# Kernel optimization log

Measured on AMD Instinct MI355X. Metric: run time of the kernel, lower is better.

## Reference

```python
import jax, jax.numpy as jnp
import numpy as np

B, C, T = 8, 1024, 2048
CI = C // 2
BN_EPS = 1e-5


def setup_inputs() -> dict:
    key = jax.random.key(0)
    ks = jax.random.split(key, 12)
    sc_in = 1.0 / np.sqrt(C)
    sc_ci = 1.0 / np.sqrt(CI)
    return {
        "x": jax.random.normal(ks[0], (B, C, T), dtype=jnp.float32),
        "Wq_w": jax.random.normal(ks[1], (CI, C), dtype=jnp.float32) * sc_in,
        "Wq_b": jax.random.normal(ks[2], (CI,), dtype=jnp.float32) * 0.02,
        "Wk_w": jax.random.normal(ks[3], (CI, C), dtype=jnp.float32) * sc_in,
        "Wk_b": jax.random.normal(ks[4], (CI,), dtype=jnp.float32) * 0.02,
        "Wv_w": jax.random.normal(ks[5], (CI, C), dtype=jnp.float32) * sc_in,
        "Wv_b": jax.random.normal(ks[6], (CI,), dtype=jnp.float32) * 0.02,
        "Wo_w": jax.random.normal(ks[7], (C, CI), dtype=jnp.float32) * sc_ci,
        "Wo_b": jax.random.normal(ks[8], (C,), dtype=jnp.float32) * 0.02,
        "gamma": jax.random.normal(ks[9], (C,), dtype=jnp.float32) * 0.1 + 1.0,
        "beta": jax.random.normal(ks[10], (C,), dtype=jnp.float32) * 0.02,
    }


def reference(x, Wq_w, Wq_b, Wk_w, Wk_b, Wv_w, Wv_b, Wo_w, Wo_b, gamma, beta):
    # 1x1 Conv1d projections == channel-wise linear maps
    q = jnp.einsum('oc,bct->bto', Wq_w, x) + Wq_b          # [B, T, Ci]
    k = jnp.einsum('oc,bct->bot', Wk_w, x) + Wk_b[:, None]  # [B, Ci, T]
    v = jnp.einsum('oc,bct->bto', Wv_w, x) + Wv_b          # [B, T, Ci]

    s = jnp.einsum('bqc,bck->bqk', q, k)                   # [B, Tq, Tk], unscaled
    sim = jax.nn.softmax(s, axis=-2)                        # softmax over QUERY axis
    y = jnp.einsum('bqk,bkc->bcq', sim, v)                  # [B, Ci, T]

    wy = jnp.einsum('oc,bct->bot', Wo_w, y) + Wo_b[:, None]  # [B, C, T]

    # BatchNorm1d in training mode: stats over (batch, time) per channel
    mean = jnp.mean(wy, axis=(0, 2), keepdims=True)
    var = jnp.var(wy, axis=(0, 2), keepdims=True)
    wy_bn = (wy - mean) * jax.lax.rsqrt(var + BN_EPS)
    wy_bn = wy_bn * gamma[None, :, None] + beta[None, :, None]

    return wy_bn + x
```

## Files before the change

kernel.cpp:

```cpp
#include <hip/hip_runtime.h>
#include <hip/hip_fp16.h>

typedef _Float16 f16;
typedef f16 f16x8 __attribute__((ext_vector_type(8)));
typedef f16 f16x4 __attribute__((ext_vector_type(4)));
typedef float f32x4 __attribute__((ext_vector_type(4)));

constexpr int Bb = 8, Cc = 1024, Tt = 2048, Ci = 512;
constexpr float BN_EPS = 1e-5f;

__device__ __forceinline__ void gload16(const f16* g, f16* l) {
  __builtin_amdgcn_global_load_lds(
      (const __attribute__((address_space(1))) void*)g,
      (__attribute__((address_space(3))) void*)l, 16, 0, 0);
}

__global__ __launch_bounds__(256)
void cvt_kernel(const float* __restrict__ src, f16* __restrict__ dst, int n4) {
  int i = blockIdx.x * blockDim.x + threadIdx.x;
  if (i < n4) {
    float4 v = *((const float4*)src + i);
    f16x4 h;
    h[0] = (f16)v.x; h[1] = (f16)v.y; h[2] = (f16)v.z; h[3] = (f16)v.w;
    *((f16x4*)dst + i) = h;
  }
}

__global__ __launch_bounds__(256)
void cvtT_kernel(const float* __restrict__ x, f16* __restrict__ xT) {
  __shared__ float tile[64][68];
  const int b = blockIdx.z, c0 = blockIdx.y * 64, t0 = blockIdx.x * 64;
  const int tid = threadIdx.x;
  const float* xp = x + ((long)b * Cc + c0) * Tt + t0;
  {
    int r = tid >> 4, c4 = (tid & 15) * 4;
    #pragma unroll
    for (int it = 0; it < 4; it++) {
      float4 v = *(const float4*)(xp + (long)(r + it * 16) * Tt + c4);
      *(float4*)&tile[r + it * 16][c4] = v;
    }
  }
  __syncthreads();
  f16* op = xT + ((long)b * Tt + t0) * Cc + c0;
  {
    int c8 = (tid & 7) * 8;
    #pragma unroll
    for (int it = 0; it < 2; it++) {
      int t = (tid >> 3) + it * 32;
      f16x8 o;
      #pragma unroll
      for (int jj = 0; jj < 8; jj++) o[jj] = (f16)tile[c8 + jj][t];
      *(f16x8*)(op + (long)t * Cc + c8) = o;
    }
  }
}

template<int BIAS_MODE, bool DO_MAX>
__device__ __forceinline__
void gemm_body(f16* lds, const f16* Ab, const f16* Bt, f16* C,
               const float* bias, unsigned* gmaxb,
               int K, int lda, int ldb, int ldc, int bm0, int bn0)
{
  constexpr int TILE_A = 256 * 32;
  constexpr int TILE_B = 128 * 32;
  constexpr int TILE   = TILE_A + TILE_B;

  const int tid = threadIdx.x, lane = tid & 63, wv = tid >> 6;
  const int wm = (wv >> 1) * 64, wn = (wv & 1) * 64;
  const int r16 = lane & 15, khi = lane >> 4;

  auto stA = [&](int slot, int k0, int r) {
    int L = (r * 512 + tid) * 16;
    int G = L ^ (((L >> 7) & 3) << 4);
    gload16(Ab + (long)(G >> 6) * lda + k0 + ((G & 63) >> 1),
            lds + (long)slot * TILE + (r * 512 + wv * 64) * 8);
  };
  auto stB = [&](int slot, int k0) {
    int L = tid * 16;
    int G = L ^ (((L >> 7) & 3) << 4);
    gload16(Bt + (long)(G >> 6) * ldb + k0 + ((G & 63) >> 1),
            lds + (long)slot * TILE + TILE_A + (wv * 64) * 8);
  };

  f32x4 acc[4][4] = {};
  const int nt = K >> 5;

  stA(0, 0, 0); stA(0, 0, 1); stB(0, 0);
  stA(1, 32, 0); stA(1, 32, 1); stB(1, 32);
  asm volatile("s_waitcnt vmcnt(3)" ::: "memory");
  __builtin_amdgcn_s_barrier();

  for (int t = 0; t < nt; t++) {
    const int slot = t % 3;
    const int nslot = (t + 2) % 3;
    const int k2 = (t + 2) << 5;
    const bool st = (t + 2) < nt;
    const char* baseA = (const char*)(lds + (long)slot * TILE);
    const char* baseB = (const char*)(lds + (long)slot * TILE + TILE_A);

    if (st) { stA(nslot, k2, 0); stA(nslot, k2, 1); stB(nslot, k2); }

    f16x8 af[4], bf[4];
    #pragma unroll
    for (int i = 0; i < 4; i++) {
      const int row = wm + i * 16 + r16;
      af[i] = *(const f16x8*)(baseA + (((row << 6) + (khi << 4)) ^ (((row >> 1) & 3) << 4)));
    }
    #pragma unroll
    for (int j = 0; j < 4; j++) {
      const int row = wn + j * 16 + r16;
      bf[j] = *(const f16x8*)(baseB + (((row << 6) + (khi << 4)) ^ (((row >> 1) & 3) << 4)));
    }

    __builtin_amdgcn_s_setprio(1);
    #pragma unroll
    for (int i = 0; i < 4; i++)
      #pragma unroll
      for (int j = 0; j < 4; j++)
        acc[i][j] = __builtin_amdgcn_mfma_f32_16x16x32_f16(af[i], bf[j], acc[i][j], 0, 0, 0);
    __builtin_amdgcn_s_setprio(0);

    __builtin_amdgcn_sched_barrier(0);
    if (st) asm volatile("s_waitcnt vmcnt(3)" ::: "memory");
    else    asm volatile("s_waitcnt vmcnt(0)" ::: "memory");
    __builtin_amdgcn_s_barrier();
  }

  const int rg = khi * 4;
  float cmx[4] = {-3e38f, -3e38f, -3e38f, -3e38f};
  #pragma unroll
  for (int i = 0; i < 4; i++) {
    const int row0 = bm0 + wm + i * 16 + rg;
    #pragma unroll
    for (int r = 0; r < 4; r++) {
      const int row = row0 + r;
      const float br = (BIAS_MODE == 1) ? bias[row] : 0.0f;
      #pragma unroll
      for (int j = 0; j < 4; j++) {
        const int col = bn0 + wn + j * 16 + r16;
        float v = acc[i][j][r] + ((BIAS_MODE == 2) ? bias[col] : br);
        C[(long)row * ldc + col] = (f16)v;
        if (DO_MAX) cmx[j] = fmaxf(cmx[j], v);
      }
    }
  }
  if (DO_MAX) {
    #pragma unroll
    for (int j = 0; j < 4; j++) {
      float mx = cmx[j];
      mx = fmaxf(mx, __shfl_xor(mx, 16));
      mx = fmaxf(mx, __shfl_xor(mx, 32));
      if (khi == 0) {
        const int col = bn0 + wn + j * 16 + r16;
        unsigned u = __float_as_uint(mx);
        unsigned key = (u & 0x80000000u) ? ~u : (u | 0x80000000u);
        atomicMax(gmaxb + col, key);
      }
    }
  }
}

template<int BIAS_MODE, bool DO_MAX>
__global__ __launch_bounds__(512, 2)
void gemm8p(const f16* __restrict__ A, const f16* __restrict__ B,
            f16* __restrict__ C, const float* __restrict__ bias,
            unsigned* __restrict__ gmax,
            int K, int lda, int ldb, int ldc, long sA, long sB, long sC,
            int nx, int ny)
{
  extern __shared__ f16 lds[];
  const int per = gridDim.x >> 3;
  const int nid = (blockIdx.x & 7) * per + (blockIdx.x >> 3);
  const int bz = nid / (nx * ny);
  const int rem = nid - bz * nx * ny;
  const int by = rem / nx, bx = rem - by * nx;
  gemm_body<BIAS_MODE, DO_MAX>(
      lds,
      A + (long)bz * sA + (long)(by * 256) * lda,
      B + (long)bz * sB + (long)(bx * 128) * ldb,
      C + (long)bz * sC, bias,
      DO_MAX ? gmax + (long)bz * ldc : nullptr,
      K, lda, ldb, ldc, by * 256, bx * 128);
}

__global__ __launch_bounds__(512, 2)
void qkv_kernel(const f16* __restrict__ xT, const f16* __restrict__ wqk,
                f16* __restrict__ QK, const float* __restrict__ qkb,
                const f16* __restrict__ wvm, f16* __restrict__ Vt,
                const float* __restrict__ Wv_b)
{
  extern __shared__ f16 lds[];
  const int per = gridDim.x >> 3;
  const int nid = (blockIdx.x & 7) * per + (blockIdx.x >> 3);
  if (nid < 512) {
    const int bz = nid >> 6, rem = nid & 63, by = rem >> 3, bx = rem & 7;
    gemm_body<2, false>(
        lds,
        xT + (long)bz * ((long)Tt * Cc) + (long)(by * 256) * Cc,
        wqk + (long)(bx * 128) * Cc,
        QK + (long)bz * ((long)Tt * 1024), qkb, nullptr,
        Cc, Cc, Cc, 1024, by * 256, bx * 128);
  } else {
    const int n2 = nid - 512;
    const int bz = n2 >> 5, rem = n2 & 31, by = rem >> 4, bx = rem & 15;
    gemm_body<1, false>(
        lds,
        wvm + (long)(by * 256) * Cc,
        xT + (long)bz * ((long)Tt * Cc) + (long)(bx * 128) * Cc,
        Vt + (long)bz * ((long)Ci * Tt), Wv_b, nullptr,
        Cc, Cc, Cc, Tt, by * 256, bx * 128);
  }
}

__global__ __launch_bounds__(256)
void colsum_kernel(f16* __restrict__ E, const unsigned* __restrict__ gmax,
                   float* __restrict__ sums) {
  const int b = blockIdx.z;
  const int kt = blockIdx.x * 256 + threadIdx.x;
  const long q0 = (long)blockIdx.y * 128;
  unsigned key = gmax[b * Tt + kt];
  float m = (key & 0x80000000u) ? __uint_as_float(key ^ 0x80000000u)
                                : __uint_as_float(~key);
  f16* p = E + ((long)b * Tt + q0) * Tt + kt;
  float s = 0.f;
  #pragma unroll 4
  for (int q = 0; q < 128; q++) {
    float e = __expf((float)p[(long)q * Tt] - m);
    p[(long)q * Tt] = (f16)e;
    s += e;
  }
  atomicAdd(sums + b * Tt + kt, s);
}

__global__ __launch_bounds__(256)
void vscale_kernel(f16* __restrict__ Vt, const float* __restrict__ sums) {
  long i = ((long)blockIdx.x * 256 + threadIdx.x) * 8;
  int kt = (int)(i & (Tt - 1));
  int b = (int)(i >> 20);
  f16x8 v = *(f16x8*)(Vt + i);
  const float* sp = sums + b * Tt + kt;
  #pragma unroll
  for (int j = 0; j < 8; j++)
    v[j] = (f16)((float)v[j] * __fdividef(1.0f, sp[j]));
  *(f16x8*)(Vt + i) = v;
}

__global__ __launch_bounds__(256)
void bnfinal_kernel(const f16* __restrict__ wy, const float* __restrict__ x,
                    const float* __restrict__ gamma, const float* __restrict__ beta,
                    float* __restrict__ out)
{
  const int c = blockIdx.x, tid = threadIdx.x;
  f16x8 w[8];
  float s1 = 0.f, s2 = 0.f;
  #pragma unroll
  for (int b = 0; b < Bb; b++) {
    w[b] = *((const f16x8*)(wy + ((long)b * Cc + c) * Tt) + tid);
    #pragma unroll
    for (int j = 0; j < 8; j++) { float f = (float)w[b][j]; s1 += f; s2 += f * f; }
  }
  #pragma unroll
  for (int off = 1; off < 64; off <<= 1) {
    s1 += __shfl_xor(s1, off);
    s2 += __shfl_xor(s2, off);
  }
  __shared__ float l1[4], l2[4];
  const int wv = tid >> 6;
  if ((tid & 63) == 0) { l1[wv] = s1; l2[wv] = s2; }
  __syncthreads();
  s1 = (l1[0] + l1[1]) + (l1[2] + l1[3]);
  s2 = (l2[0] + l2[1]) + (l2[2] + l2[3]);
  const float cnt = (float)Bb * (float)Tt;
  const float mean = s1 / cnt;
  const float var  = s2 / cnt - mean * mean;
  const float sc = rsqrtf(var + BN_EPS) * gamma[c];
  const float sh = beta[c] - mean * sc;
  #pragma unroll
  for (int b = 0; b < Bb; b++) {
    const long base = ((long)b * Cc + c) * Tt + tid * 8;
    float4 x0 = *(const float4*)(x + base);
    float4 x1 = *(const float4*)(x + base + 4);
    float4 o0, o1;
    o0.x = (float)w[b][0] * sc + sh + x0.x;
    o0.y = (float)w[b][1] * sc + sh + x0.y;
    o0.z = (float)w[b][2] * sc + sh + x0.z;
    o0.w = (float)w[b][3] * sc + sh + x0.w;
    o1.x = (float)w[b][4] * sc + sh + x1.x;
    o1.y = (float)w[b][5] * sc + sh + x1.y;
    o1.z = (float)w[b][6] * sc + sh + x1.z;
    o1.w = (float)w[b][7] * sc + sh + x1.w;
    *(float4*)(out + base)     = o0;
    *(float4*)(out + base + 4) = o1;
  }
}

extern "C" void kernel_launch(void* const* d_in, const int* in_sizes, int n_in,
                              void* d_out, int out_size, void* d_ws, size_t ws_size,
                              hipStream_t stream) {
  const float* x    = (const float*)d_in[0];
  const float* Wq_w = (const float*)d_in[1];
  const float* Wq_b = (const float*)d_in[2];
  const float* Wk_w = (const float*)d_in[3];
  const float* Wk_b = (const float*)d_in[4];
  const float* Wv_w = (const float*)d_in[5];
  const float* Wv_b = (const float*)d_in[6];
  const float* Wo_w = (const float*)d_in[7];
  const float* Wo_b = (const float*)d_in[8];
  const float* gamma = (const float*)d_in[9];
  const float* beta  = (const float*)d_in[10];
  float* out = (float*)d_out;

  constexpr long SZ_XT = (long)Bb * Tt * Cc;
  constexpr long SZ_Q  = (long)Bb * Tt * Ci;
  constexpr long SZ_S  = (long)Bb * Tt * Tt;
  constexpr long SZ_W  = (long)Ci * Cc;

  f16* ws = (f16*)d_ws;
  f16* xT  = ws;
  f16* QK  = xT + SZ_XT;
  f16* Vt  = QK + SZ_XT;
  f16* Sq  = Vt + SZ_Q;
  f16* Y   = Sq + SZ_S;
  f16* wy  = Y + SZ_Q;
  f16* wqk = wy + SZ_XT;
  f16* wv  = wqk + 2 * SZ_W;
  f16* wo  = wv + SZ_W;
  unsigned* gmax = (unsigned*)(wo + SZ_W);
  float* sums = (float*)(gmax + (long)Bb * Tt);
  float* qkb  = sums + (long)Bb * Tt;

  constexpr int LDSB = (256 * 32 + 128 * 32) * 3 * 2;
  hipFuncSetAttribute(reinterpret_cast<const void*>(qkv_kernel),
                      hipFuncAttributeMaxDynamicSharedMemorySize, LDSB);
  hipFuncSetAttribute(reinterpret_cast<const void*>(gemm8p<0, true>),
                      hipFuncAttributeMaxDynamicSharedMemorySize, LDSB);
  hipFuncSetAttribute(reinterpret_cast<const void*>(gemm8p<0, false>),
                      hipFuncAttributeMaxDynamicSharedMemorySize, LDSB);
  hipFuncSetAttribute(reinterpret_cast<const void*>(gemm8p<1, false>),
                      hipFuncAttributeMaxDynamicSharedMemorySize, LDSB);

  hipMemsetAsync(gmax, 0, (long)Bb * Tt * 2 * sizeof(float), stream);
  hipMemcpyAsync(qkb, Wq_b, Ci * sizeof(float), hipMemcpyDeviceToDevice, stream);
  hipMemcpyAsync(qkb + Ci, Wk_b, Ci * sizeof(float), hipMemcpyDeviceToDevice, stream);

  cvt_kernel<<<(int)(SZ_W / 4 / 256), 256, 0, stream>>>(Wq_w, wqk, (int)(SZ_W / 4));
  cvt_kernel<<<(int)(SZ_W / 4 / 256), 256, 0, stream>>>(Wk_w, wqk + SZ_W, (int)(SZ_W / 4));
  cvt_kernel<<<(int)(SZ_W / 4 / 256), 256, 0, stream>>>(Wv_w, wv, (int)(SZ_W / 4));
  cvt_kernel<<<(int)(SZ_W / 4 / 256), 256, 0, stream>>>(Wo_w, wo, (int)(SZ_W / 4));
  cvtT_kernel<<<dim3(Tt / 64, Cc / 64, Bb), 256, 0, stream>>>(x, xT);

  qkv_kernel<<<768, 512, LDSB, stream>>>(xT, wqk, QK, qkb, wv, Vt, Wv_b);

  gemm8p<0, true><<<16 * 8 * Bb, 512, LDSB, stream>>>(
      QK, QK + 512, Sq, nullptr, gmax,
      Ci, 1024, 1024, Tt, (long)Tt * 1024, (long)Tt * 1024, (long)Tt * Tt, 16, 8);

  colsum_kernel<<<dim3(Tt / 256, Tt / 128, Bb), 256, 0, stream>>>(Sq, gmax, sums);

  vscale_kernel<<<(int)(SZ_Q / 8 / 256), 256, 0, stream>>>(Vt, sums);

  gemm8p<0, false><<<4 * 8 * Bb, 512, LDSB, stream>>>(
      Sq, Vt, Y, nullptr, nullptr,
      Tt, Tt, Tt, Ci, (long)Tt * Tt, (long)Ci * Tt, (long)Tt * Ci, 4, 8);

  gemm8p<1, false><<<16 * 4 * Bb, 512, LDSB, stream>>>(
      wo, Y, wy, Wo_b, nullptr,
      Ci, Ci, Ci, Tt, 0, (long)Tt * Ci, (long)Cc * Tt, 16, 4);

  bnfinal_kernel<<<Cc, 256, 0, stream>>>(wy, x, gamma, beta, out);
}
```

Before: 267.9 us.

## Co-schedule V projection GEMM with column-sum exp pass in one launch

Moves the V projection GEMM out of the combined QKV launch and into a new kernel that also runs the memory-bound exp/column-sum pass over the score matrix. Q/K projection now runs alone as a plain batched GEMM. The aim is to overlap compute-bound V GEMM blocks with bandwidth-bound colsum blocks so both resources stay busy. The colsum blocks now use 512 threads and carry the GEMM's LDS allocation and launch bounds, which may lower their occupancy.

```diff
diff --git a/kernel.cpp b/kernel.cpp
--- a/kernel.cpp
+++ b/kernel.cpp
@@ -184,52 +184,41 @@
 }
 
 __global__ __launch_bounds__(512, 2)
-void qkv_kernel(const f16* __restrict__ xT, const f16* __restrict__ wqk,
-                f16* __restrict__ QK, const float* __restrict__ qkb,
-                const f16* __restrict__ wvm, f16* __restrict__ Vt,
-                const float* __restrict__ Wv_b)
+void vcol_kernel(const f16* __restrict__ xT, const f16* __restrict__ wvm,
+                 f16* __restrict__ Vt, const float* __restrict__ Wv_b,
+                 f16* __restrict__ E, const unsigned* __restrict__ gmax,
+                 float* __restrict__ sums)
 {
   extern __shared__ f16 lds[];
   const int per = gridDim.x >> 3;
   const int nid = (blockIdx.x & 7) * per + (blockIdx.x >> 3);
-  if (nid < 512) {
-    const int bz = nid >> 6, rem = nid & 63, by = rem >> 3, bx = rem & 7;
-    gemm_body<2, false>(
-        lds,
-        xT + (long)bz * ((long)Tt * Cc) + (long)(by * 256) * Cc,
-        wqk + (long)(bx * 128) * Cc,
-        QK + (long)bz * ((long)Tt * 1024), qkb, nullptr,
-        Cc, Cc, Cc, 1024, by * 256, bx * 128);
-  } else {
-    const int n2 = nid - 512;
-    const int bz = n2 >> 5, rem = n2 & 31, by = rem >> 4, bx = rem & 15;
+  if (nid < 256) {
+    const int bz = nid >> 5, rem = nid & 31, by = rem >> 4, bx = rem & 15;
     gemm_body<1, false>(
         lds,
         wvm + (long)(by * 256) * Cc,
         xT + (long)bz * ((long)Tt * Cc) + (long)(bx * 128) * Cc,
         Vt + (long)bz * ((long)Ci * Tt), Wv_b, nullptr,
         Cc, Cc, Cc, Tt, by * 256, bx * 128);
-  }
-}
-
-__global__ __launch_bounds__(256)
-void colsum_kernel(f16* __restrict__ E, const unsigned* __restrict__ gmax,
-                   float* __restrict__ sums) {
-  const int b = blockIdx.z;
-  const int kt = blockIdx.x * 256 + threadIdx.x;
-  const long q0 = (long)blockIdx.y * 128;
-  unsigned key = gmax[b * Tt + kt];
-  float m = (key & 0x80000000u) ? __uint_as_float(key ^ 0x80000000u)
-                                : __uint_as_float(~key);
-  f16* p = E + ((long)b * Tt + q0) * Tt + kt;
-  float s = 0.f;
-  #pragma unroll 4
-  for (int q = 0; q < 128; q++) {
-    float e = __expf((float)p[(long)q * Tt] - m);
-    p[(long)q * Tt] = (f16)e;
-    s += e;
-  }
-  atomicAdd(sums + b * Tt + kt, s);
+  } else {
+    const int cid = nid - 256;
+    const int b = cid >> 6, rem = cid & 63;
+    const int xk = rem >> 4, yq = rem & 15;
+    const int kt = xk * 512 + threadIdx.x;
+    const long q0 = (long)yq * 128;
+    unsigned key = gmax[b * Tt + kt];
+    float m = (key & 0x80000000u) ? __uint_as_float(key ^ 0x80000000u)
+                                  : __uint_as_float(~key);
+    f16* p = E + ((long)b * Tt + q0) * Tt + kt;
+    float s = 0.f;
+    #pragma unroll 4
+    for (int q = 0; q < 128; q++) {
+      float e = __expf((float)p[(long)q * Tt] - m);
+      p[(long)q * Tt] = (f16)e;
+      s += e;
+    }
+    atomicAdd(sums + b * Tt + kt, s);
+  }
 }
 
 __global__ __launch_bounds__(256)
@@ -330,7 +319,9 @@
   float* qkb  = sums + (long)Bb * Tt;
 
   constexpr int LDSB = (256 * 32 + 128 * 32) * 3 * 2;
-  hipFuncSetAttribute(reinterpret_cast<const void*>(qkv_kernel),
+  hipFuncSetAttribute(reinterpret_cast<const void*>(gemm8p<2, false>),
+                      hipFuncAttributeMaxDynamicSharedMemorySize, LDSB);
+  hipFuncSetAttribute(reinterpret_cast<const void*>(vcol_kernel),
                       hipFuncAttributeMaxDynamicSharedMemorySize, LDSB);
   hipFuncSetAttribute(reinterpret_cast<const void*>(gemm8p<0, true>),
                       hipFuncAttributeMaxDynamicSharedMemorySize, LDSB);
@@ -349,13 +340,15 @@
   cvt_kernel<<<(int)(SZ_W / 4 / 256), 256, 0, stream>>>(Wo_w, wo, (int)(SZ_W / 4));
   cvtT_kernel<<<dim3(Tt / 64, Cc / 64, Bb), 256, 0, stream>>>(x, xT);
 
-  qkv_kernel<<<768, 512, LDSB, stream>>>(xT, wqk, QK, qkb, wv, Vt, Wv_b);
+  gemm8p<2, false><<<8 * 8 * Bb, 512, LDSB, stream>>>(
+      xT, wqk, QK, qkb, nullptr,
+      Cc, Cc, Cc, 1024, (long)Tt * Cc, 0, (long)Tt * 1024, 8, 8);
 
   gemm8p<0, true><<<16 * 8 * Bb, 512, LDSB, stream>>>(
       QK, QK + 512, Sq, nullptr, gmax,
       Ci, 1024, 1024, Tt, (long)Tt * 1024, (long)Tt * 1024, (long)Tt * Tt, 16, 8);
 
-  colsum_kernel<<<dim3(Tt / 256, Tt / 128, Bb), 256, 0, stream>>>(Sq, gmax, sums);
+  vcol_kernel<<<768, 512, LDSB, stream>>>(xT, wv, Vt, Wv_b, Sq, gmax, sums);
 
   vscale_kernel<<<(int)(SZ_Q / 8 / 256), 256, 0, stream>>>(Vt, sums);
 
```

Result: slower. 284.2 us (+6.1%).
